# Kernel optimization log

Hardware: AMD Instinct MI355X
Metric: run time of the kernel (lower is better)

## Reference

```python
import jax, jax.numpy as jnp
import numpy as np

DROPOUT_RATE = 0.1  # init arg dropout_rate
B, D, N_SEL = 4096, 4096, 2048


def setup_inputs() -> dict:
    key = jax.random.key(0)
    k1, k2 = jax.random.split(key)
    inputs = jax.random.normal(k1, (B, D), dtype=jnp.float32)
    neuron_indices = jax.random.randint(k2, (N_SEL,), 0, D, dtype=jnp.int32)
    return {"inputs": inputs, "neuron_indices": neuron_indices}


def reference(inputs, neuron_indices):
    # Training-mode SelectiveDropout: for each listed neuron (column), draw an
    # independent uniform; drop the column (0) with prob p, else scale by 1/(1-p).
    # Unlisted columns keep scale 1. Vectorized replacement for the per-index
    # torch.rand(1) loop.
    key = jax.random.key(42)
    u = jax.random.uniform(key, neuron_indices.shape, dtype=jnp.float32)
    keep_scale = jnp.where(u < DROPOUT_RATE, 0.0, 1.0 / (1.0 - DROPOUT_RATE))
    scale = jnp.ones((inputs.shape[1],), dtype=inputs.dtype)
    scale = scale.at[neuron_indices].set(keep_scale.astype(inputs.dtype))
    return inputs * scale[None, :]
```

## Files before the change

kernel.cpp:

```cpp
#include <hip/hip_runtime.h>
#include <stdint.h>


#define D_DIM 4096

typedef float f32x4 __attribute__((ext_vector_type(4)));
typedef int i32x4 __attribute__((ext_vector_type(4)));

__device__ __forceinline__ uint32_t rotl32(uint32_t v, uint32_t n) {
  return (v << n) | (v >> (32u - n));
}

__device__ __forceinline__ void threefry2x32(uint32_t x0, uint32_t x1,
                                             uint32_t& o0, uint32_t& o1) {
  const uint32_t ks0 = 0u;
  const uint32_t ks1 = 42u;
  const uint32_t ks2 = 0u ^ 42u ^ 0x1BD11BDAu;

  x0 += ks0;
  x1 += ks1;

#define TF_GROUP(a, b, c, d)                           \
  x0 += x1; x1 = rotl32(x1, a); x1 ^= x0;              \
  x0 += x1; x1 = rotl32(x1, b); x1 ^= x0;              \
  x0 += x1; x1 = rotl32(x1, c); x1 ^= x0;              \
  x0 += x1; x1 = rotl32(x1, d); x1 ^= x0;

  TF_GROUP(13, 15, 26, 6)  x0 += ks1; x1 += ks2 + 1u;
  TF_GROUP(17, 29, 16, 24) x0 += ks2; x1 += ks0 + 2u;
  TF_GROUP(13, 15, 26, 6)  x0 += ks0; x1 += ks1 + 3u;
  TF_GROUP(17, 29, 16, 24) x0 += ks1; x1 += ks2 + 4u;
  TF_GROUP(13, 15, 26, 6)  x0 += ks2; x1 += ks0 + 5u;
#undef TF_GROUP

  o0 = x0;
  o1 = x1;
}

__device__ __forceinline__ int keep_bit(int i) {
  uint32_t o0, o1;
  threefry2x32(0u, (uint32_t)i, o0, o1);
  uint32_t bits = o0 ^ o1;
  float u = __uint_as_float((bits >> 9) | 0x3F800000u) - 1.0f;
  return (u < 0.1f) ? 0 : 1;
}

__global__ __launch_bounds__(256) void selective_dropout_fused(
    const f32x4* __restrict__ in, const int* __restrict__ idx, int n,
    f32x4* __restrict__ out, int total4) {
  __shared__ int packed[D_DIM];
  const int t = threadIdx.x;
  const int tid = blockIdx.x * 256 + t;
  const int stride = gridDim.x * 256;
  const float inv_keep = (float)(1.0 / (1.0 - 0.1));
  i32x4* p4 = (i32x4*)packed;

  if (n == 2048 && total4 == stride * 8) {
    i32x4 c0 = *(const i32x4*)&idx[t * 8];
    i32x4 c1 = *(const i32x4*)&idx[t * 8 + 4];
    __builtin_amdgcn_sched_barrier(0);

    f32x4 v[8];
#pragma unroll
    for (int k = 0; k < 8; ++k) v[k] = in[tid + k * stride];

#pragma unroll
    for (int k = 0; k < 4; ++k) {
      i32x4 m1;
      m1[0] = -1; m1[1] = -1; m1[2] = -1; m1[3] = -1;
      p4[t + k * 256] = m1;
    }
    asm volatile("s_waitcnt lgkmcnt(0)" ::: "memory");
    __builtin_amdgcn_s_barrier();

#pragma unroll
    for (int k = 0; k < 8; ++k) {
      int i = t * 8 + k;
      int col = (k < 4) ? c0[k] : c1[k - 4];
      atomicMax(&packed[col], (i << 1) | keep_bit(i));
    }
    asm volatile("s_waitcnt lgkmcnt(0)" ::: "memory");
    __builtin_amdgcn_s_barrier();

    i32x4 pk = p4[tid & 1023];
    f32x4 s;
#pragma unroll
    for (int j = 0; j < 4; ++j)
      s[j] = (pk[j] < 0) ? 1.0f : ((pk[j] & 1) ? inv_keep : 0.0f);

#pragma unroll
    for (int k = 0; k < 8; ++k) {
      v[k] *= s;
      out[tid + k * stride] = v[k];
    }
  } else {
    for (int d = t; d < D_DIM; d += 256) packed[d] = -1;
    __syncthreads();
    for (int i = t; i < n; i += 256) {
      atomicMax(&packed[idx[i]], (i << 1) | keep_bit(i));
    }
    __syncthreads();
    for (int e = tid; e < total4; e += stride) {
      i32x4 pk = p4[e & (D_DIM / 4 - 1)];
      f32x4 s;
#pragma unroll
      for (int j = 0; j < 4; ++j)
        s[j] = (pk[j] < 0) ? 1.0f : ((pk[j] & 1) ? inv_keep : 0.0f);
      f32x4 x = in[e];
      x *= s;
      out[e] = x;
    }
  }
}

extern "C" void kernel_launch(void* const* d_in, const int* in_sizes, int n_in,
                              void* d_out, int out_size, void* d_ws, size_t ws_size,
                              hipStream_t stream) {
  const float* in = (const float*)d_in[0];
  const int* idx = (const int*)d_in[1];
  float* out = (float*)d_out;

  const int n_idx = in_sizes[1];
  const int total = in_sizes[0];
  const int total4 = total / 4;

  const int blocks = 2048;
  hipLaunchKernelGGL(selective_dropout_fused, dim3(blocks), dim3(256), 0,
                     stream, (const f32x4*)in, idx, n_idx, (f32x4*)out,
                     total4);
}
```

Measured before the change: 28.82 us.

## Filter indices to each block's column quarter before computing dropout bits

```diff
diff --git a/kernel.cpp b/kernel.cpp
--- a/kernel.cpp
+++ b/kernel.cpp
@@ -48,14 +48,18 @@
 __global__ __launch_bounds__(256) void selective_dropout_fused(
     const f32x4* __restrict__ in, const int* __restrict__ idx, int n,
     f32x4* __restrict__ out, int total4) {
-  __shared__ int packed[D_DIM];
+  __shared__ int lds[D_DIM];
   const int t = threadIdx.x;
   const int tid = blockIdx.x * 256 + t;
   const int stride = gridDim.x * 256;
   const float inv_keep = (float)(1.0 / (1.0 - 0.1));
-  i32x4* p4 = (i32x4*)packed;
 
   if (n == 2048 && total4 == stride * 8) {
+    int* packed = lds;
+    int* comp = lds + 1024;
+    int* cnt = lds + 3072;
+    const int q = blockIdx.x & 3;
+
     i32x4 c0 = *(const i32x4*)&idx[t * 8];
     i32x4 c1 = *(const i32x4*)&idx[t * 8 + 4];
     __builtin_amdgcn_sched_barrier(0);
@@ -63,26 +67,47 @@
     f32x4 v[8];
 #pragma unroll
     for (int k = 0; k < 8; ++k) v[k] = in[tid + k * stride];
+    __builtin_amdgcn_sched_barrier(0);
 
-#pragma unroll
-    for (int k = 0; k < 4; ++k) {
+    {
       i32x4 m1;
       m1[0] = -1; m1[1] = -1; m1[2] = -1; m1[3] = -1;
-      p4[t + k * 256] = m1;
+      ((i32x4*)packed)[t] = m1;
+    }
+    if (t == 0) *cnt = 0;
+    asm volatile("s_waitcnt lgkmcnt(0)" ::: "memory");
+    __builtin_amdgcn_s_barrier();
+
+    const int lane = t & 63;
+    const unsigned long long lt_mask = (lane == 0) ? 0ull : (~0ull >> (64 - lane));
+#pragma unroll
+    for (int k = 0; k < 8; ++k) {
+      int i = t * 8 + k;
+      int d = (k < 4) ? c0[k] : c1[k - 4];
+      bool match = ((d >> 10) == q);
+      unsigned long long mask = __ballot(match);
+      int base = 0;
+      if (lane == 0) base = atomicAdd(cnt, __popcll(mask));
+      base = __shfl(base, 0);
+      if (match) {
+        int prefix = __popcll(mask & lt_mask);
+        comp[base + prefix] = (i << 12) | d;
+      }
     }
     asm volatile("s_waitcnt lgkmcnt(0)" ::: "memory");
     __builtin_amdgcn_s_barrier();
 
-#pragma unroll
-    for (int k = 0; k < 8; ++k) {
-      int i = t * 8 + k;
-      int col = (k < 4) ? c0[k] : c1[k - 4];
-      atomicMax(&packed[col], (i << 1) | keep_bit(i));
+    int m = *cnt;
+    for (int j = t; j < m; j += 256) {
+      int e = comp[j];
+      int i = e >> 12;
+      int d = e & 4095;
+      atomicMax(&packed[d & 1023], (i << 1) | keep_bit(i));
     }
     asm volatile("s_waitcnt lgkmcnt(0)" ::: "memory");
     __builtin_amdgcn_s_barrier();
 
-    i32x4 pk = p4[tid & 1023];
+    i32x4 pk = ((i32x4*)packed)[t];
     f32x4 s;
 #pragma unroll
     for (int j = 0; j < 4; ++j)
@@ -94,6 +119,7 @@
       out[tid + k * stride] = v[k];
     }
   } else {
+    int* packed = lds;
     for (int d = t; d < D_DIM; d += 256) packed[d] = -1;
     __syncthreads();
     for (int i = t; i < n; i += 256) {
@@ -101,7 +127,7 @@
     }
     __syncthreads();
     for (int e = tid; e < total4; e += stride) {
-      i32x4 pk = p4[e & (D_DIM / 4 - 1)];
+      i32x4 pk = ((i32x4*)packed)[e & (D_DIM / 4 - 1)];
       f32x4 s;
 #pragma unroll
       for (int j = 0; j < 4; ++j)
```

Result: faster. 28.08 us (-2.6%).
